# Performance work log

Hardware: AMD Instinct MI355X
Metric: run time of the kernel (lower is better)

## Reference

```python
import jax, jax.numpy as jnp
import numpy as np

TAU = 0.1

def setup_inputs() -> dict:
    key = jax.random.key(0)
    kZ, k1, k2 = jax.random.split(key, 3)
    N, D = 8192, 128
    scale = 1.0 / np.sqrt(D)
    return {
        "Z": jax.random.normal(kZ, (N, D), dtype=jnp.float32),
        "W1": jax.random.normal(k1, (D, D), dtype=jnp.float32) * scale,
        "b1": jnp.zeros((D,), dtype=jnp.float32),
        "W2": jax.random.normal(k2, (D, D), dtype=jnp.float32) * scale,
        "b2": jnp.zeros((D,), dtype=jnp.float32),
    }

def reference(Z, W1, b1, W2, b2):
    # DiffusivityTransform: 2-layer MLP with ReLU (torch Linear: x @ W.T + b;
    # here W1/W2 are stored already transposed as [in, out])
    t = jax.nn.relu(Z @ W1 + b1) @ W2 + b2          # [N, D]
    sim = t @ t.T                                     # [N, N]
    S = jax.nn.softmax(sim, axis=1)                   # row-stochastic [N, N]
    Z_prop = S @ Z                                    # [N, D]
    return Z + TAU * (Z_prop - Z)
```

## Files before the change

kernel.cpp:

```cpp
#include <hip/hip_runtime.h>

typedef _Float16 half_t;
typedef _Float16 hx8 __attribute__((ext_vector_type(8)));
typedef _Float16 hx4 __attribute__((ext_vector_type(4)));
typedef float fx4 __attribute__((ext_vector_type(4)));

#define LOG2E 1.44269504088896f
#define TAU 0.1f
#define NSPLIT 8

__global__ __launch_bounds__(256) void mlpz_kernel(
    const float* __restrict__ Z, const float* __restrict__ W1,
    const float* __restrict__ b1, const float* __restrict__ W2,
    const float* __restrict__ b2, half_t* __restrict__ T,
    half_t* __restrict__ Zth)
{
  __shared__ float Ztile[16*132];
  __shared__ half_t Hs[16*136];
  const int tid = threadIdx.x;
  const int w = tid >> 6, lane = tid & 63;
  const int q = lane >> 4, c = lane & 15;
  const int rb = blockIdx.x*16;

#pragma unroll
  for (int i=0;i<2;++i) {
    int fid = i*256 + tid;
    int r = fid >> 5, c4 = (fid & 31)*4;
    *(fx4*)(&Ztile[r*132 + c4]) = *(const fx4*)(Z + (size_t)(rb + r)*128 + c4);
  }
  __syncthreads();

  {
    const int d = tid & 127, h = tid >> 7;
    hx8 hv;
#pragma unroll
    for (int u=0;u<8;++u) hv[u] = (half_t)Ztile[(h*8 + u)*132 + d];
    *(hx8*)(Zth + (size_t)d*8192 + rb + h*8) = hv;
  }

  hx8 zb[4];
#pragma unroll
  for (int ks=0;ks<4;++ks) {
    fx4 a = *(const fx4*)(&Ztile[c*132 + ks*32 + q*8]);
    fx4 b = *(const fx4*)(&Ztile[c*132 + ks*32 + q*8 + 4]);
#pragma unroll
    for (int u=0;u<4;++u) { zb[ks][u] = (half_t)a[u]; zb[ks][4+u] = (half_t)b[u]; }
  }

#pragma unroll
  for (int m2=0;m2<2;++m2) {
    const int mt = w*2 + m2;
    fx4 acc = (fx4){0.f,0.f,0.f,0.f};
#pragma unroll
    for (int ks=0;ks<4;++ks) {
      hx8 aw;
#pragma unroll
      for (int j=0;j<8;++j)
        aw[j] = (half_t)W1[(size_t)(ks*32 + q*8 + j)*128 + mt*16 + c];
      acc = __builtin_amdgcn_mfma_f32_16x16x32_f16(aw, zb[ks], acc, 0,0,0);
    }
    fx4 bias = *(const fx4*)(b1 + mt*16 + 4*q);
    hx4 hv;
#pragma unroll
    for (int i=0;i<4;++i) {
      float h = acc[i] + bias[i];
      hv[i] = (half_t)(h > 0.f ? h : 0.f);
    }
    *(hx4*)(&Hs[c*136 + mt*16 + 4*q]) = hv;
  }
  __syncthreads();

  hx8 hb[4];
#pragma unroll
  for (int ks=0;ks<4;++ks) hb[ks] = *(const hx8*)(&Hs[c*136 + ks*32 + q*8]);
#pragma unroll
  for (int m2=0;m2<2;++m2) {
    const int mt = w*2 + m2;
    fx4 acc = (fx4){0.f,0.f,0.f,0.f};
#pragma unroll
    for (int ks=0;ks<4;++ks) {
      hx8 aw;
#pragma unroll
      for (int j=0;j<8;++j)
        aw[j] = (half_t)W2[(size_t)(ks*32 + q*8 + j)*128 + mt*16 + c];
      acc = __builtin_amdgcn_mfma_f32_16x16x32_f16(aw, hb[ks], acc, 0,0,0);
    }
    fx4 bias = *(const fx4*)(b2 + mt*16 + 4*q);
    hx4 tv;
#pragma unroll
    for (int i=0;i<4;++i) tv[i] = (half_t)(acc[i] + bias[i]);
    *(hx4*)(T + (size_t)(rb + c)*128 + mt*16 + 4*q) = tv;
  }
}

__global__ __launch_bounds__(256,2) void flash_kernel(
    const half_t* __restrict__ T, const half_t* __restrict__ Zt,
    half_t* __restrict__ Pacc, float* __restrict__ Pm, float* __restrict__ Pl)
{
  __shared__ half_t Tbuf[2][8*512];
  __shared__ half_t Zbuf[2][8*512];
  const int tid = threadIdx.x;
  const int w = tid >> 6, lane = tid & 63;
  const int q = lane >> 4, c = lane & 15;
  const int bx = blockIdx.x;
  const int qb = bx >> 3, kh = bx & 7;
  const int wrow = qb*64 + w*16;
  const int sw = (c & 7) * 8;

  hx8 bq[4];
#pragma unroll
  for (int ks=0;ks<4;++ks)
    bq[ks] = *(const hx8*)(T + (size_t)(wrow + c)*128 + ks*32 + q*8);

  fx4 oacc[8];
#pragma unroll
  for (int mtd=0;mtd<8;++mtd) oacc[mtd] = (fx4){0.f,0.f,0.f,0.f};
  float m_run = -1e30f;
  float l_run = 0.f;

  const int kbase = kh*1024;

  auto issue_loads = [&](int kt0, int b) {
    if (w < 2) {
#pragma unroll
      for (int i=0;i<4;++i) {
        int f = w*4 + i, mt = f >> 2, ks = f & 3;
        const half_t* gp = T + (size_t)(kt0 + mt*16 + c)*128 + ks*32 + q*8;
        half_t* lp = &Tbuf[b][f*512 + lane*8];
        __builtin_amdgcn_global_load_lds(
            (const __attribute__((address_space(1))) void*)gp,
            (__attribute__((address_space(3))) void*)lp, 16, 0, 0);
      }
    } else {
#pragma unroll
      for (int i=0;i<4;++i) {
        int f2 = (w-2)*4 + i;
        const half_t* gp = Zt + (size_t)(f2*16 + c)*8192 + kt0 + q*8;
        half_t* lp = &Zbuf[b][f2*512 + lane*8];
        __builtin_amdgcn_global_load_lds(
            (const __attribute__((address_space(1))) void*)gp,
            (__attribute__((address_space(3))) void*)lp, 16, 0, 0);
      }
    }
  };

  issue_loads(kbase, 0);

  for (int t=0;t<32;++t) {
    const int cur = t & 1;
    __syncthreads();
    half_t* Tcur = Tbuf[cur];
    half_t* Zcur = Zbuf[cur];
    half_t* Psw  = &Tbuf[cur][w*1024];

    fx4 sacc[2];
#pragma unroll
    for (int mt=0;mt<2;++mt) sacc[mt] = (fx4){0.f,0.f,0.f,0.f};
    __builtin_amdgcn_s_setprio(1);
#pragma unroll
    for (int ks=0;ks<4;++ks)
#pragma unroll
      for (int mt=0;mt<2;++mt) {
        hx8 ak = *(const hx8*)(&Tcur[(mt*4+ks)*512 + lane*8]);
        sacc[mt] = __builtin_amdgcn_mfma_f32_16x16x32_f16(ak, bq[ks], sacc[mt], 0,0,0);
      }
    __builtin_amdgcn_s_setprio(0);

    float mx = -1e30f;
#pragma unroll
    for (int mt=0;mt<2;++mt)
#pragma unroll
      for (int i=0;i<4;++i) mx = fmaxf(mx, sacc[mt][i]);
    mx = fmaxf(mx, __shfl_xor(mx, 16, 64));
    mx = fmaxf(mx, __shfl_xor(mx, 32, 64));
    float mnew = fmaxf(m_run, mx);
    float alpha = __builtin_amdgcn_exp2f((m_run - mnew)*LOG2E);
    m_run = mnew;
    float nb = mnew*LOG2E;
    float rs = 0.f;
    hx4 pk[2];
#pragma unroll
    for (int mt=0;mt<2;++mt)
#pragma unroll
      for (int i=0;i<4;++i) {
        float p = __builtin_amdgcn_exp2f(sacc[mt][i]*LOG2E - nb);
        rs += p;
        pk[mt][i] = (half_t)p;
      }
    rs += __shfl_xor(rs, 16, 64);
    rs += __shfl_xor(rs, 32, 64);
    l_run = l_run*alpha + rs;
#pragma unroll
    for (int mtd=0;mtd<8;++mtd)
#pragma unroll
      for (int i=0;i<4;++i) oacc[mtd][i] *= alpha;

    __syncthreads();
    if (t < 31) issue_loads(kbase + (t+1)*32, cur ^ 1);

#pragma unroll
    for (int mt=0;mt<2;++mt)
      *(hx4*)(&Psw[c*64 + ((mt*16 + 4*q) ^ sw)]) = pk[mt];

    {
      hx8 bp = *(const hx8*)(&Psw[c*64 + ((q*8) ^ sw)]);
      __builtin_amdgcn_s_setprio(1);
#pragma unroll
      for (int mtd=0;mtd<8;++mtd) {
        hx8 az = *(const hx8*)(&Zcur[mtd*512 + lane*8]);
        oacc[mtd] = __builtin_amdgcn_mfma_f32_16x16x32_f16(az, bp, oacc[mtd], 0,0,0);
      }
      __builtin_amdgcn_s_setprio(0);
    }
  }

  float inv = 1.0f / l_run;
  const size_t prow = (size_t)(((qb >> 1)*8 + kh)*128 + (qb & 1)*64 + w*16 + c);
#pragma unroll
  for (int mtd=0;mtd<8;++mtd) {
    hx4 ov;
#pragma unroll
    for (int i=0;i<4;++i) ov[i] = (half_t)(oacc[mtd][i]*inv);
    *(hx4*)(Pacc + prow*128 + mtd*16 + 4*q) = ov;
  }
  if (q == 0) {
    Pm[prow] = m_run;
    Pl[prow] = l_run;
  }
}

__global__ __launch_bounds__(256) void merge_kernel(
    const float* __restrict__ Z, const half_t* __restrict__ Pacc,
    const float* __restrict__ Pm, const float* __restrict__ Pl,
    float* __restrict__ out)
{
  const int th = blockIdx.x*256 + threadIdx.x;
  const int r = th >> 5, cg = th & 31;
  const int qb = r >> 7, rr = r & 127;
  float mk[NSPLIT], lk[NSPLIT];
  float M = -1e30f;
#pragma unroll
  for (int k=0;k<NSPLIT;++k) {
    int p = qb*NSPLIT + k;
    mk[k] = Pm[p*128 + rr];
    lk[k] = Pl[p*128 + rr];
    M = fmaxf(M, mk[k]);
  }
  float L = 0.f, wk[NSPLIT];
#pragma unroll
  for (int k=0;k<NSPLIT;++k) { wk[k] = lk[k]*__builtin_amdgcn_exp2f((mk[k]-M)*LOG2E); L += wk[k]; }
  float o0=0.f,o1=0.f,o2=0.f,o3=0.f;
#pragma unroll
  for (int k=0;k<NSPLIT;++k) {
    int p = qb*NSPLIT + k;
    hx4 v = *(const hx4*)(Pacc + ((size_t)p*128 + rr)*128 + cg*4);
    o0 += wk[k]*(float)v[0]; o1 += wk[k]*(float)v[1];
    o2 += wk[k]*(float)v[2]; o3 += wk[k]*(float)v[3];
  }
  float invL = 1.0f / L;
  fx4 zv = *(const fx4*)(Z + (size_t)r*128 + cg*4);
  fx4 res;
  res[0] = (1.f-TAU)*zv[0] + TAU*o0*invL;
  res[1] = (1.f-TAU)*zv[1] + TAU*o1*invL;
  res[2] = (1.f-TAU)*zv[2] + TAU*o2*invL;
  res[3] = (1.f-TAU)*zv[3] + TAU*o3*invL;
  *(fx4*)(out + (size_t)r*128 + cg*4) = res;
}

extern "C" void kernel_launch(void* const* d_in, const int* in_sizes, int n_in,
                              void* d_out, int out_size, void* d_ws, size_t ws_size,
                              hipStream_t stream) {
  const float* Z  = (const float*)d_in[0];
  const float* W1 = (const float*)d_in[1];
  const float* b1 = (const float*)d_in[2];
  const float* W2 = (const float*)d_in[3];
  const float* b2 = (const float*)d_in[4];
  float* out = (float*)d_out;

  char* ws = (char*)d_ws;
  const size_t NBLK = 64 * NSPLIT;
  half_t* Thi  = (half_t*)(ws);
  half_t* Zth  = (half_t*)(ws + (size_t)2*1024*1024);
  half_t* Pacc = (half_t*)(ws + (size_t)4*1024*1024);
  float*  Pm   = (float*)(ws + (size_t)4*1024*1024 + NBLK*128*128*2);
  float*  Pl   = Pm + NBLK*128;

  hipLaunchKernelGGL(mlpz_kernel,  dim3(512),  dim3(256), 0, stream, Z, W1, b1, W2, b2, Thi, Zth);
  hipLaunchKernelGGL(flash_kernel, dim3(128*NSPLIT), dim3(256), 0, stream, Thi, Zth, Pacc, Pm, Pl);
  hipLaunchKernelGGL(merge_kernel, dim3(1024), dim3(256), 0, stream, Z, Pacc, Pm, Pl, out);
}
```

Measured before the change: 144.8 us.

## Pre-pack fp16 weights, widen flash key tile, load Z directly to registers

A new small kernel converts W1 and W2 to fp16 and packs them into MFMA fragment order, so the MLP kernel reads one vector per fragment instead of eight strided fp32 loads. The flash kernel now processes 64 keys per iteration instead of 32, halving loop trips and barriers. Z^T fragments are loaded straight from global memory into registers rather than staged through LDS. The P tile moves to a separate per-wave LDS buffer, which removes the second __syncthreads. The Zth transpose store mapping is also changed to improve coalescing. The costs are an extra kernel launch, more register pressure from holding the Z fragments, and more global-load latency that must be hidden.

New measurement: 227.7 us. 57.3% more time.

```diff
diff --git a/kernel.cpp b/kernel.cpp
--- a/kernel.cpp
+++ b/kernel.cpp
@@ -9,9 +9,28 @@
 #define TAU 0.1f
 #define NSPLIT 8
 
+__global__ __launch_bounds__(256) void wpack_kernel(
+    const float* __restrict__ W1, const float* __restrict__ W2,
+    half_t* __restrict__ Wh1, half_t* __restrict__ Wh2)
+{
+  const int job = blockIdx.x*256 + threadIdx.x;
+  const int lane = job & 63;
+  const int frag = (job >> 6) & 31;
+  const int mat  = job >> 11;
+  const int mt = frag >> 2, ks = frag & 3;
+  const int q = lane >> 4, c = lane & 15;
+  const float* W = mat ? W2 : W1;
+  half_t* Wh = mat ? Wh2 : Wh1;
+  hx8 v;
+#pragma unroll
+  for (int j=0;j<8;++j)
+    v[j] = (half_t)W[(size_t)(ks*32 + q*8 + j)*128 + mt*16 + c];
+  *(hx8*)(Wh + ((size_t)frag*64 + lane)*8) = v;
+}
+
 __global__ __launch_bounds__(256) void mlpz_kernel(
-    const float* __restrict__ Z, const float* __restrict__ W1,
-    const float* __restrict__ b1, const float* __restrict__ W2,
+    const float* __restrict__ Z, const half_t* __restrict__ Wh1,
+    const float* __restrict__ b1, const half_t* __restrict__ Wh2,
     const float* __restrict__ b2, half_t* __restrict__ T,
     half_t* __restrict__ Zth)
 {
@@ -31,7 +50,7 @@
   __syncthreads();
 
   {
-    const int d = tid & 127, h = tid >> 7;
+    const int d = tid >> 1, h = tid & 1;
     hx8 hv;
 #pragma unroll
     for (int u=0;u<8;++u) hv[u] = (half_t)Ztile[(h*8 + u)*132 + d];
@@ -53,10 +72,7 @@
     fx4 acc = (fx4){0.f,0.f,0.f,0.f};
 #pragma unroll
     for (int ks=0;ks<4;++ks) {
-      hx8 aw;
-#pragma unroll
-      for (int j=0;j<8;++j)
-        aw[j] = (half_t)W1[(size_t)(ks*32 + q*8 + j)*128 + mt*16 + c];
+      hx8 aw = *(const hx8*)(Wh1 + ((size_t)(mt*4 + ks)*64 + lane)*8);
       acc = __builtin_amdgcn_mfma_f32_16x16x32_f16(aw, zb[ks], acc, 0,0,0);
     }
     fx4 bias = *(const fx4*)(b1 + mt*16 + 4*q);
@@ -79,10 +95,7 @@
     fx4 acc = (fx4){0.f,0.f,0.f,0.f};
 #pragma unroll
     for (int ks=0;ks<4;++ks) {
-      hx8 aw;
-#pragma unroll
-      for (int j=0;j<8;++j)
-        aw[j] = (half_t)W2[(size_t)(ks*32 + q*8 + j)*128 + mt*16 + c];
+      hx8 aw = *(const hx8*)(Wh2 + ((size_t)(mt*4 + ks)*64 + lane)*8);
       acc = __builtin_amdgcn_mfma_f32_16x16x32_f16(aw, hb[ks], acc, 0,0,0);
     }
     fx4 bias = *(const fx4*)(b2 + mt*16 + 4*q);
@@ -97,8 +110,8 @@
     const half_t* __restrict__ T, const half_t* __restrict__ Zt,
     half_t* __restrict__ Pacc, float* __restrict__ Pm, float* __restrict__ Pl)
 {
-  __shared__ half_t Tbuf[2][8*512];
-  __shared__ half_t Zbuf[2][8*512];
+  __shared__ half_t Tbuf[2][16*512];
+  __shared__ half_t Pbuf[4][16*64];
   const int tid = threadIdx.x;
   const int w = tid >> 6, lane = tid & 63;
   const int q = lane >> 4, c = lane & 15;
@@ -119,102 +132,97 @@
   float l_run = 0.f;
 
   const int kbase = kh*1024;
+  half_t* Psw = &Pbuf[w][0];
 
   auto issue_loads = [&](int kt0, int b) {
-    if (w < 2) {
-#pragma unroll
-      for (int i=0;i<4;++i) {
-        int f = w*4 + i, mt = f >> 2, ks = f & 3;
-        const half_t* gp = T + (size_t)(kt0 + mt*16 + c)*128 + ks*32 + q*8;
-        half_t* lp = &Tbuf[b][f*512 + lane*8];
-        __builtin_amdgcn_global_load_lds(
-            (const __attribute__((address_space(1))) void*)gp,
-            (__attribute__((address_space(3))) void*)lp, 16, 0, 0);
-      }
-    } else {
-#pragma unroll
-      for (int i=0;i<4;++i) {
-        int f2 = (w-2)*4 + i;
-        const half_t* gp = Zt + (size_t)(f2*16 + c)*8192 + kt0 + q*8;
-        half_t* lp = &Zbuf[b][f2*512 + lane*8];
-        __builtin_amdgcn_global_load_lds(
-            (const __attribute__((address_space(1))) void*)gp,
-            (__attribute__((address_space(3))) void*)lp, 16, 0, 0);
-      }
+#pragma unroll
+    for (int i=0;i<4;++i) {
+      int f = w*4 + i, mt = f >> 2, ks = f & 3;
+      const half_t* gp = T + (size_t)(kt0 + mt*16 + c)*128 + ks*32 + q*8;
+      half_t* lp = &Tbuf[b][f*512 + lane*8];
+      __builtin_amdgcn_global_load_lds(
+          (const __attribute__((address_space(1))) void*)gp,
+          (__attribute__((address_space(3))) void*)lp, 16, 0, 0);
     }
   };
 
   issue_loads(kbase, 0);
 
-  for (int t=0;t<32;++t) {
+  for (int t=0;t<16;++t) {
     const int cur = t & 1;
     __syncthreads();
+
+    const half_t* zbase = Zt + (size_t)c*8192 + kbase + t*64 + q*8;
+    hx8 az[8][2];
+#pragma unroll
+    for (int mtd=0;mtd<8;++mtd)
+#pragma unroll
+      for (int ks2=0;ks2<2;++ks2)
+        az[mtd][ks2] = *(const hx8*)(zbase + (size_t)mtd*16*8192 + ks2*32);
+    __builtin_amdgcn_sched_barrier(0);
+
+    if (t < 15) issue_loads(kbase + (t+1)*64, cur ^ 1);
+    __builtin_amdgcn_sched_barrier(0);
+
     half_t* Tcur = Tbuf[cur];
-    half_t* Zcur = Zbuf[cur];
-    half_t* Psw  = &Tbuf[cur][w*1024];
-
-    fx4 sacc[2];
-#pragma unroll
-    for (int mt=0;mt<2;++mt) sacc[mt] = (fx4){0.f,0.f,0.f,0.f};
-    __builtin_amdgcn_s_setprio(1);
+
+    fx4 sacc[4];
+#pragma unroll
+    for (int mt=0;mt<4;++mt) sacc[mt] = (fx4){0.f,0.f,0.f,0.f};
 #pragma unroll
     for (int ks=0;ks<4;++ks)
 #pragma unroll
-      for (int mt=0;mt<2;++mt) {
+      for (int mt=0;mt<4;++mt) {
         hx8 ak = *(const hx8*)(&Tcur[(mt*4+ks)*512 + lane*8]);
         sacc[mt] = __builtin_amdgcn_mfma_f32_16x16x32_f16(ak, bq[ks], sacc[mt], 0,0,0);
       }
-    __builtin_amdgcn_s_setprio(0);
-
-    float mx = -1e30f;
-#pragma unroll
-    for (int mt=0;mt<2;++mt)
-#pragma unroll
-      for (int i=0;i<4;++i) mx = fmaxf(mx, sacc[mt][i]);
-    mx = fmaxf(mx, __shfl_xor(mx, 16, 64));
-    mx = fmaxf(mx, __shfl_xor(mx, 32, 64));
-    float mnew = fmaxf(m_run, mx);
-    float alpha = __builtin_amdgcn_exp2f((m_run - mnew)*LOG2E);
-    m_run = mnew;
-    float nb = mnew*LOG2E;
-    float rs = 0.f;
-    hx4 pk[2];
-#pragma unroll
-    for (int mt=0;mt<2;++mt)
-#pragma unroll
-      for (int i=0;i<4;++i) {
-        float p = __builtin_amdgcn_exp2f(sacc[mt][i]*LOG2E - nb);
-        rs += p;
-        pk[mt][i] = (half_t)p;
+
+    {
+      float a0 = fmaxf(fmaxf(sacc[0][0], sacc[0][1]), sacc[0][2]);
+      float a1 = fmaxf(fmaxf(sacc[0][3], sacc[1][0]), sacc[1][1]);
+      float a2 = fmaxf(fmaxf(sacc[1][2], sacc[1][3]), sacc[2][0]);
+      float a3 = fmaxf(fmaxf(sacc[2][1], sacc[2][2]), sacc[2][3]);
+      float a4 = fmaxf(fmaxf(sacc[3][0], sacc[3][1]), sacc[3][2]);
+      float mx = fmaxf(fmaxf(fmaxf(a0, a1), fmaxf(a2, a3)),
+                       fmaxf(a4, sacc[3][3]));
+      mx = fmaxf(mx, __shfl_xor(mx, 16, 64));
+      mx = fmaxf(mx, __shfl_xor(mx, 32, 64));
+      float mnew = fmaxf(m_run, mx);
+      float alpha = __builtin_amdgcn_exp2f((m_run - mnew)*LOG2E);
+      m_run = mnew;
+      float nb = mnew*LOG2E;
+      float rs = 0.f;
+#pragma unroll
+      for (int mt=0;mt<4;++mt) {
+        hx4 pkv;
+#pragma unroll
+        for (int i=0;i<4;++i) {
+          float p = __builtin_amdgcn_exp2f(sacc[mt][i]*LOG2E - nb);
+          rs += p;
+          pkv[i] = (half_t)p;
+        }
+        *(hx4*)(&Psw[c*64 + ((mt*16 + 4*q) ^ sw)]) = pkv;
       }
-    rs += __shfl_xor(rs, 16, 64);
-    rs += __shfl_xor(rs, 32, 64);
-    l_run = l_run*alpha + rs;
-#pragma unroll
-    for (int mtd=0;mtd<8;++mtd)
-#pragma unroll
-      for (int i=0;i<4;++i) oacc[mtd][i] *= alpha;
-
-    __syncthreads();
-    if (t < 31) issue_loads(kbase + (t+1)*32, cur ^ 1);
-
-#pragma unroll
-    for (int mt=0;mt<2;++mt)
-      *(hx4*)(&Psw[c*64 + ((mt*16 + 4*q) ^ sw)]) = pk[mt];
-
-    {
-      hx8 bp = *(const hx8*)(&Psw[c*64 + ((q*8) ^ sw)]);
-      __builtin_amdgcn_s_setprio(1);
-#pragma unroll
-      for (int mtd=0;mtd<8;++mtd) {
-        hx8 az = *(const hx8*)(&Zcur[mtd*512 + lane*8]);
-        oacc[mtd] = __builtin_amdgcn_mfma_f32_16x16x32_f16(az, bp, oacc[mtd], 0,0,0);
-      }
-      __builtin_amdgcn_s_setprio(0);
-    }
-  }
-
-  float inv = 1.0f / l_run;
+      l_run = l_run*alpha + rs;
+#pragma unroll
+      for (int mtd=0;mtd<8;++mtd)
+#pragma unroll
+        for (int i=0;i<4;++i) oacc[mtd][i] *= alpha;
+    }
+
+#pragma unroll
+    for (int ks2=0;ks2<2;++ks2) {
+      hx8 bp = *(const hx8*)(&Psw[c*64 + ((ks2*32 + q*8) ^ sw)]);
+#pragma unroll
+      for (int mtd=0;mtd<8;++mtd)
+        oacc[mtd] = __builtin_amdgcn_mfma_f32_16x16x32_f16(az[mtd][ks2], bp, oacc[mtd], 0,0,0);
+    }
+  }
+
+  float lf = l_run;
+  lf += __shfl_xor(lf, 16, 64);
+  lf += __shfl_xor(lf, 32, 64);
+  float inv = 1.0f / lf;
   const size_t prow = (size_t)(((qb >> 1)*8 + kh)*128 + (qb & 1)*64 + w*16 + c);
 #pragma unroll
   for (int mtd=0;mtd<8;++mtd) {
@@ -225,7 +233,7 @@
   }
   if (q == 0) {
     Pm[prow] = m_run;
-    Pl[prow] = l_run;
+    Pl[prow] = lf;
   }
 }
 
@@ -284,8 +292,11 @@
   half_t* Pacc = (half_t*)(ws + (size_t)4*1024*1024);
   float*  Pm   = (float*)(ws + (size_t)4*1024*1024 + NBLK*128*128*2);
   float*  Pl   = Pm + NBLK*128;
-
-  hipLaunchKernelGGL(mlpz_kernel,  dim3(512),  dim3(256), 0, stream, Z, W1, b1, W2, b2, Thi, Zth);
+  half_t* Wh1  = (half_t*)(ws + (size_t)20*1024*1024 + 512*1024);
+  half_t* Wh2  = Wh1 + 32*64*8;
+
+  hipLaunchKernelGGL(wpack_kernel, dim3(16),   dim3(256), 0, stream, W1, W2, Wh1, Wh2);
+  hipLaunchKernelGGL(mlpz_kernel,  dim3(512),  dim3(256), 0, stream, Z, Wh1, b1, Wh2, b2, Thi, Zth);
   hipLaunchKernelGGL(flash_kernel, dim3(128*NSPLIT), dim3(256), 0, stream, Thi, Zth, Pacc, Pm, Pl);
   hipLaunchKernelGGL(merge_kernel, dim3(1024), dim3(256), 0, stream, Z, Pacc, Pm, Pl, out);
 }
```
